# Kernel optimization log

Hardware: AMD Instinct MI355X
Metric: run time of the kernel (lower is better)

## Reference

```python
import jax, jax.numpy as jnp
import numpy as np

D = 4          # subsample stride for quantized refs
R = 6          # local search radius
P = 2 * R + 1  # 13
N = P * P      # 169
C = 32         # one-hot classes
BETA = 50.0
SIG = 1.0      # gaussian kernel sigma for kernel_soft_argmax
MPR = 12       # memory_patch_R
MPP = 2 * MPR + 1  # 25
DIL_INT = 15


def bilinear_gather(img, ys, xs):
    # img (b,c,h,w); ys,xs (b,n,h,w) float pixel coords; zero padding outside.
    b, c, h, w = img.shape
    y0f = jnp.floor(ys); x0f = jnp.floor(xs)
    wy = ys - y0f; wx = xs - x0f
    y0 = y0f.astype(jnp.int32); x0 = x0f.astype(jnp.int32)
    imgf = img.reshape(b, c, h * w)

    def corner(yi, xi, wgt):
        valid = (yi >= 0) & (yi < h) & (xi >= 0) & (xi < w)
        idx = jnp.clip(yi, 0, h - 1) * w + jnp.clip(xi, 0, w - 1)  # (b,n,h,w)
        g = jax.vmap(lambda f, ix: f[:, ix])(imgf, idx)            # (b,c,n,h,w)
        return g * (wgt * valid)[:, None]

    return (corner(y0, x0, (1 - wy) * (1 - wx))
            + corner(y0, x0 + 1, (1 - wy) * wx)
            + corner(y0 + 1, x0, wy * (1 - wx))
            + corner(y0 + 1, x0 + 1, wy * wx))


def deform_im2col(img, offset):
    # img (b,c,h,w); offset (b,h,w,2) ordered (dx,dy); returns (b,c,N,h,w)
    b, c, h, w = img.shape
    n = jnp.arange(N)
    dy = (n // P - R).astype(jnp.float32)
    dx = (n % P - R).astype(jnp.float32)
    yy = jnp.arange(h, dtype=jnp.float32)[:, None]
    xx = jnp.arange(w, dtype=jnp.float32)[None, :]
    ys = yy[None, None] + offset[..., 1][:, None] + dy[None, :, None, None]
    xs = xx[None, None] + offset[..., 0][:, None] + dx[None, :, None, None]
    return bilinear_gather(img, ys, xs)


def local_corr(t, r, rad, dil):
    # SpatialCorrelationSampler(kernel_size=1, patch_size=2*rad+1, dilation_patch=dil)
    pad = rad * dil
    rp = jnp.pad(r, ((0, 0), (0, 0), (pad, pad), (pad, pad)))
    offs = jnp.arange(2 * rad + 1) * dil

    def dot(oy, ox):
        rs = jax.lax.dynamic_slice(rp, (0, 0, oy, ox), t.shape)
        return jnp.sum(t * rs, axis=1)  # (b,h,w)

    f = jax.vmap(lambda oy: jax.vmap(lambda ox: dot(oy, ox))(offs))(offs)  # (Pp,Pp,b,h,w)
    return jnp.transpose(f, (2, 0, 1, 3, 4))  # (b,Pp,Pp,h,w), axis1=dy, axis2=dx


def unfold(x, ksz, pad):
    # torch F.unfold: (b,c,h,w) -> (b,c,ksz*ksz,h*w), n = ky*ksz+kx, zero pad
    b, c, h, w = x.shape
    xp = jnp.pad(x, ((0, 0), (0, 0), (pad, pad), (pad, pad)))
    offs = jnp.arange(ksz)
    sl = jax.vmap(lambda oy: jax.vmap(
        lambda ox: jax.lax.dynamic_slice(xp, (0, 0, oy, ox), x.shape))(offs))(offs)
    return jnp.transpose(sl, (2, 3, 0, 1, 4, 5)).reshape(b, c, ksz * ksz, h * w)


def kernel_soft_argmax(corr):
    # corr (B, N, h, w): gaussian-weight then softmax(beta * .) over N
    k = jnp.arange(P, dtype=jnp.float32)
    ctr = (P - 1) / 2.0
    g = jnp.exp(-(((k[None, :] - ctr) ** 2) + ((k[:, None] - ctr) ** 2)) / (2 * SIG ** 2))
    return jax.nn.softmax(BETA * (g.reshape(1, N, 1, 1) * corr), axis=1)


def get_grid(corr):
    # corr (B, N, h, w) -> soft-argmax grid (B, h, w, 2) in normalized coords
    B, n, h, w = corr.shape
    # replicate the torch meshgrid variable swap in the original get_grid
    x_map = jnp.broadcast_to(jnp.linspace(-1.0, 1.0, w)[None, :], (h, w)).astype(jnp.float32)
    y_map = jnp.broadcast_to(jnp.linspace(-1.0, 1.0, h)[:, None], (h, w)).astype(jnp.float32)
    xg = unfold(x_map[None, None], P, R)[:, 0]  # (1,N,hw)
    yg = unfold(y_map[None, None], P, R)[:, 0]
    wgt = corr.reshape(B, n, h * w)
    wgt = wgt / jnp.sum(wgt, 1, keepdims=True)
    gx = (wgt * xg).sum(1).reshape(B, h, w, 1)
    gy = (wgt * yg).sum(1).reshape(B, h, w, 1)
    return jnp.concatenate([gx, gy], 3)


def forward(feats_r, feats_t, quantized_r, ref_index, current_ind):
    ref_list = [int(v) for v in np.asarray(ref_index)]  # static config
    cur = int(current_ind)
    nref = feats_r.shape[0]
    nsearch = len([x for x in ref_list if cur - x > DIL_INT])
    dirates = [min(4, (cur - x) // DIL_INT + 1) for x in ref_list if cur - x > DIL_INT]
    b, c, h, w = feats_t.shape

    mdy = jnp.arange(-MPR, MPR + 1, dtype=jnp.float32)
    corrs, offsets = [], []
    for si in range(nsearch):
        cc = local_corr(feats_t, feats_r[si], MPR, dirates[si])       # (b,25,25,h,w)
        cc = jax.nn.softmax(cc.reshape(b, MPP * MPP, h * w), axis=1)
        cc = cc.reshape(b, MPP, MPP, h, w)
        offx = jnp.einsum('bpqhw,q->bhw', cc, mdy)   # expectation of dx
        offy = jnp.einsum('bpqhw,p->bhw', cc, mdy)   # expectation of dy
        off = jnp.stack([offx, offy], -1) * float(dirates[si])        # (b,h,w,2)
        offsets.append(off)
        col0 = deform_im2col(feats_r[si], off)                        # (b,c,N,h,w)
        corrs.append(jnp.einsum('bchw,bcnhw->bnhw', feats_t, col0))
    for ind in range(nsearch, nref):
        corrs.append(local_corr(feats_t, feats_r[ind], R, 1).reshape(b, N, h, w))

    corr = jnp.concatenate(corrs, 0)                 # (b*nref, N, h, w)
    corr = kernel_soft_argmax(corr)
    corr = corr.reshape(b, 1, N * nref, h * w)
    grid = get_grid(corr.reshape(-1, N, h, w))       # (b*nref, h, w, 2)

    # prep: subsample ::D and one-hot single-channel label maps
    labels = quantized_r[:, :, 0, ::D, ::D]          # (nref, b, h, w)
    qr = (labels[:, :, None] == jnp.arange(C)[None, None, :, None, None]).astype(jnp.float32)

    cols = []
    for i in range(nsearch):
        cols.append(deform_im2col(qr[i], offsets[i]).reshape(b, C, N, h * w))
    for i in range(nsearch, nref):
        cols.append(unfold(qr[i], P, R))
    image_uf = jnp.concatenate(cols, 2)              # (b, C, N*nref, hw)

    out = jnp.einsum('bnl,bcnl->bcl', corr[:, 0], image_uf).reshape(b, C, h, w)
    return out, grid


def setup_inputs() -> dict:
    key = jax.random.key(0)
    k1, k2, k3 = jax.random.split(key, 3)
    feats_r = jax.random.normal(k1, (3, 1, 64, 64, 64), dtype=jnp.float32)
    feats_t = jax.random.normal(k2, (1, 64, 64, 64), dtype=jnp.float32)
    quantized_r = jax.random.randint(k3, (3, 1, 1, 256, 256), 0, C, dtype=jnp.int32)
    return {
        'feats_r': feats_r,
        'feats_t': feats_t,
        'quantized_r': quantized_r,
        'ref_index': np.arange(3),
        'current_ind': 16,
    }


def reference(feats_r, feats_t, quantized_r, ref_index, current_ind):
    return forward(feats_r, feats_t, quantized_r, ref_index, current_ind)
```

## Files before the change

kernel.cpp:

```cpp
#include <hip/hip_runtime.h>


#define NPIX 4096

__device__ __forceinline__ float pdot8(float4 t0, float4 t1, float4 a,
                                       float4 b) {
  float s0 = t0.x * a.x, s1 = t0.y * a.y, s2 = t0.z * a.z, s3 = t0.w * a.w;
  s0 = fmaf(t1.x, b.x, s0);
  s1 = fmaf(t1.y, b.y, s1);
  s2 = fmaf(t1.z, b.z, s2);
  s3 = fmaf(t1.w, b.w, s3);
  return (s0 + s1) + (s2 + s3);
}

__device__ __forceinline__ float red8_8(float p0, float p1, float p2,
                                        float p3, float p4, float p5,
                                        float p6, float p7, int tx) {
  bool o1 = tx & 1, o2 = tx & 2, o4 = tx & 4;
  float a = (o1 ? p1 : p0) + __shfl_xor(o1 ? p0 : p1, 1);
  float b = (o1 ? p3 : p2) + __shfl_xor(o1 ? p2 : p3, 1);
  float c = (o1 ? p5 : p4) + __shfl_xor(o1 ? p4 : p5, 1);
  float d = (o1 ? p7 : p6) + __shfl_xor(o1 ? p6 : p7, 1);
  float e = (o2 ? b : a) + __shfl_xor(o2 ? a : b, 2);
  float f = (o2 ? d : c) + __shfl_xor(o2 ? c : d, 2);
  return (o4 ? f : e) + __shfl_xor(o4 ? e : f, 4);
}

__device__ __forceinline__ float red8(float v) {
  v += __shfl_xor(v, 1);
  v += __shfl_xor(v, 2);
  v += __shfl_xor(v, 4);
  return v;
}

__device__ __forceinline__ float wredmax(float v) {
#pragma unroll
  for (int o = 32; o; o >>= 1) v = fmaxf(v, __shfl_down(v, o));
  return __shfl(v, 0);
}
__device__ __forceinline__ float wredsum(float v) {
#pragma unroll
  for (int o = 32; o; o >>= 1) v += __shfl_down(v, o);
  return __shfl(v, 0);
}

__global__ __launch_bounds__(256) void k_transpose(
    const float* __restrict__ ft, const float* __restrict__ fr,
    const int* __restrict__ q, float* __restrict__ tT, float* __restrict__ rT,
    unsigned char* __restrict__ lblp) {
  __shared__ float tile[64][65];
  int img = blockIdx.y;
  int pixBase = blockIdx.x * 64;
  const float* src = (img == 0) ? ft : fr + (img - 1) * (64 * NPIX);
  float* dst = (img == 0) ? tT : rT + (img - 1) * (64 * NPIX);
  int tid = threadIdx.x;
#pragma unroll
  for (int it = 0; it < 4; ++it) {
    int idx = it * 256 + tid;
    int c = idx >> 4;
    int p4 = (idx & 15) << 2;
    float4 v = *(const float4*)&src[c * NPIX + pixBase + p4];
    tile[p4 + 0][c] = v.x;
    tile[p4 + 1][c] = v.y;
    tile[p4 + 2][c] = v.z;
    tile[p4 + 3][c] = v.w;
  }
  __syncthreads();
#pragma unroll
  for (int it = 0; it < 4; ++it) {
    int idx = it * 256 + tid;
    int p = idx >> 4;
    int c4 = (idx & 15) << 2;
    float4 v = make_float4(tile[p][c4], tile[p][c4 + 1], tile[p][c4 + 2],
                           tile[p][c4 + 3]);
    *(float4*)&dst[(pixBase + p) * 64 + c4] = v;
  }
  if (img >= 1 && tid < 64) {
    int pix = pixBase + tid;
    lblp[(img - 1) * 4096 + pix] = (unsigned char)
        q[(img - 1) * 65536 + (pix >> 6) * 1024 + (pix & 63) * 4];
  }
}

__global__ __launch_bounds__(512, 4) void k_fused(
    const float* __restrict__ tT, const float* __restrict__ rT,
    const unsigned char* __restrict__ lblp, float* __restrict__ out,
    float* __restrict__ grid) {
  int xg = blockIdx.x, y = blockIdx.y, z = blockIdx.z;
  int x0 = (xg >> 1) * 16 + (xg & 1);
  int tid = threadIdx.x;
  int g8 = tid >> 3, tx = tid & 7;
  int w = tid >> 6, lane = tid & 63;

  __shared__ float cc1[8 * 636];
  __shared__ float D[8][196];
  __shared__ float P0[8][169];
  __shared__ float bins[8][33];

  if (tid < 264) ((float*)bins)[tid] = 0.f;

  const float4* tb = (const float4*)&tT[((y << 6) + x0) << 6];
  float4 t0a = tb[0 * 32 + 2 * tx], t0b = tb[0 * 32 + 2 * tx + 1];
  float4 t1a = tb[1 * 32 + 2 * tx], t1b = tb[1 * 32 + 2 * tx + 1];
  float4 t2a = tb[2 * 32 + 2 * tx], t2b = tb[2 * 32 + 2 * tx + 1];
  float4 t3a = tb[3 * 32 + 2 * tx], t3b = tb[3 * 32 + 2 * tx + 1];
  float4 t4a = tb[4 * 32 + 2 * tx], t4b = tb[4 * 32 + 2 * tx + 1];
  float4 t5a = tb[5 * 32 + 2 * tx], t5b = tb[5 * 32 + 2 * tx + 1];
  float4 t6a = tb[6 * 32 + 2 * tx], t6b = tb[6 * 32 + 2 * tx + 1];
  float4 t7a = tb[7 * 32 + 2 * tx], t7b = tb[7 * 32 + 2 * tx + 1];

  if (z == 0) {
    {
      int u = g8 & 31, oyb = g8 >> 5;
      int rx = x0 - 24 + 2 * u;
      bool cok = (unsigned)rx < 64u;
      int colB = min(max(rx, 0), 63) * 64 + tx * 8;
      int ox = u - tx;
      bool sok = (unsigned)ox < 25u;
#pragma unroll 4
      for (int r = 0; r < 13; ++r) {
        int oy = oyb + 2 * r;
        int ry = y + 2 * oy - 24;
        bool ok = cok & (oy < 25) & ((unsigned)ry < 64u);
        const float4* rp =
            (const float4*)&rT[min(max(ry, 0), 63) * 4096 + colB];
        float4 ra = rp[0], rb = rp[1];
        float v = red8_8(pdot8(t0a, t0b, ra, rb), pdot8(t1a, t1b, ra, rb),
                         pdot8(t2a, t2b, ra, rb), pdot8(t3a, t3b, ra, rb),
                         pdot8(t4a, t4b, ra, rb), pdot8(t5a, t5b, ra, rb),
                         pdot8(t6a, t6b, ra, rb), pdot8(t7a, t7b, ra, rb),
                         tx);
        v = ok ? v : 0.f;
        if (sok && (oy < 25)) cc1[tx * 636 + oy * 25 + ox] = v;
      }
    }
    __syncthreads();

    float offx, offy;
    {
      float vv[10];
      float m = -3e38f;
#pragma unroll
      for (int it = 0; it < 10; ++it) {
        unsigned o = lane + (it << 6);
        float v = (o < 625u) ? cc1[w * 636 + o] : -3e38f;
        vv[it] = v;
        m = fmaxf(m, v);
      }
      m = wredmax(m);
      float s = 0.f, sx = 0.f, sy = 0.f;
#pragma unroll
      for (int it = 0; it < 10; ++it) {
        unsigned o = lane + (it << 6);
        unsigned oy = o / 25u, ox = o - oy * 25u;
        float e = __expf(vv[it] - m);
        s += e;
        sx += e * (float)((int)ox - 12);
        sy += e * (float)((int)oy - 12);
      }
      s = wredsum(s);
      sx = wredsum(sx);
      sy = wredsum(sy);
      offx = 2.f * sx / s;
      offy = 2.f * sy / s;
    }

    float fy = floorf(offy), fx = floorf(offx);
    float wy = offy - fy, wx = offx - fx;
    float w00 = (1.f - wy) * (1.f - wx), w01 = (1.f - wy) * wx;
    float w10 = wy * (1.f - wx), w11 = wy * wx;
    int iy0 = y + (int)fy - 6;
    int ix0 = x0 + 2 * w + (int)fx - 6;

    {
      const float4* Tp = (const float4*)&tT[((y << 6) + x0 + 2 * w) << 6];
      float4 T0 = Tp[2 * tx], T1 = Tp[2 * tx + 1];
      int g3 = lane >> 3;
#pragma unroll 4
      for (int r = 0; r < 28; ++r) {
        int idx = g3 + (r << 3);
        int a = idx >> 4, b = idx & 15;
        int ry = iy0 + a, rx = ix0 + b;
        bool ok = (b < 14) & ((unsigned)ry < 64u) & ((unsigned)rx < 64u);
        const float4* rp = (const float4*)
            &rT[(min(max(ry, 0), 63) * 64 + min(max(rx, 0), 63)) * 64];
        float4 ra = rp[2 * tx], rb = rp[2 * tx + 1];
        float v = red8(pdot8(T0, T1, ra, rb));
        if (tx == 0 && b < 14) D[w][a * 14 + b] = ok ? v : 0.f;
      }
    }

    {
      int px = x0 + 2 * w, pix = (y << 6) + px;
      float sc[3];
      float m = -3e38f;
#pragma unroll
      for (int it = 0; it < 3; ++it) {
        unsigned o = lane + (it << 6);
        float scv = -3e38f;
        if (o < 169u) {
          unsigned i = o / 13u, j = o - i * 13u;
          float v = w00 * D[w][i * 14 + j] + w01 * D[w][i * 14 + j + 1] +
                    w10 * D[w][(i + 1) * 14 + j] +
                    w11 * D[w][(i + 1) * 14 + j + 1];
          float di = (float)(((int)i - 6) * ((int)i - 6) +
                             ((int)j - 6) * ((int)j - 6));
          scv = 50.f * __expf(-0.5f * di) * v;
        }
        sc[it] = scv;
        m = fmaxf(m, scv);
      }
      m = wredmax(m);
      float ee[3];
      float s = 0.f, gx = 0.f, gy = 0.f;
#pragma unroll
      for (int it = 0; it < 3; ++it) {
        unsigned o = lane + (it << 6);
        unsigned i = o / 13u, j = o - i * 13u;
        float e = __expf(sc[it] - m);
        ee[it] = e;
        int yy = y + (int)i - 6, xx = px + (int)j - 6;
        bool inb = (o < 169u) && (unsigned)yy < 64u && (unsigned)xx < 64u;
        s += e;
        gx += e * (inb ? (-1.f + (2.f / 63.f) * (float)xx) : 0.f);
        gy += e * (inb ? (-1.f + (2.f / 63.f) * (float)yy) : 0.f);
      }
      s = wredsum(s);
      gx = wredsum(gx);
      gy = wredsum(gy);
      float invS = 1.f / s;
#pragma unroll
      for (int it = 0; it < 3; ++it) {
        unsigned o = lane + (it << 6);
        if (o < 169u) P0[w][o] = ee[it] * invS;
      }
      if (lane == 0) {
        grid[pix * 2 + 0] = gx * invS;
        grid[pix * 2 + 1] = gy * invS;
      }
    }

    {
#pragma unroll
      for (int it = 0; it < 4; ++it) {
        int idx = lane + (it << 6);
        int a = idx >> 4, b = idx & 15;
        if (a < 14 && b < 14) {
          int ry = iy0 + a, rx = ix0 + b;
          if ((unsigned)ry < 64u && (unsigned)rx < 64u) {
            float wgt = 0.f;
            const float* crp = P0[w];
            if (a < 13) {
              if (b < 13) wgt = fmaf(w00, crp[a * 13 + b], wgt);
              if (b > 0) wgt = fmaf(w01, crp[a * 13 + b - 1], wgt);
            }
            if (a > 0) {
              if (b < 13) wgt = fmaf(w10, crp[(a - 1) * 13 + b], wgt);
              if (b > 0) wgt = fmaf(w11, crp[(a - 1) * 13 + b - 1], wgt);
            }
            if (wgt != 0.f) atomicAdd(&bins[w][lblp[ry * 64 + rx]], wgt);
          }
        }
      }
    }
    __syncthreads();
  } else {
    int k = z;
    const float* rb0 = rT + (k << 18);
    float (*cc2)[169] = (float(*)[169])cc1;
    {
      int u = g8 & 31, ib = g8 >> 5;
      int rx = x0 - 6 + u;
      bool cok = (unsigned)rx < 64u;
      int colB = min(max(rx, 0), 63) * 64 + tx * 8;
      int j = u - 2 * tx;
      bool sok = (unsigned)j < 13u;
#pragma unroll 4
      for (int r = 0; r < 7; ++r) {
        int i = ib + 2 * r;
        int ry = y + i - 6;
        bool ok = cok & (i < 13) & ((unsigned)ry < 64u);
        const float4* rp =
            (const float4*)&rb0[min(max(ry, 0), 63) * 4096 + colB];
        float4 ra = rp[0], rb = rp[1];
        float v = red8_8(pdot8(t0a, t0b, ra, rb), pdot8(t1a, t1b, ra, rb),
                         pdot8(t2a, t2b, ra, rb), pdot8(t3a, t3b, ra, rb),
                         pdot8(t4a, t4b, ra, rb), pdot8(t5a, t5b, ra, rb),
                         pdot8(t6a, t6b, ra, rb), pdot8(t7a, t7b, ra, rb),
                         tx);
        v = ok ? v : 0.f;
        if (sok && (i < 13)) cc2[tx][i * 13 + j] = v;
      }
    }
    __syncthreads();
    {
      int px = x0 + 2 * w, pix = (y << 6) + px;
      float sc[3];
      float m = -3e38f;
#pragma unroll
      for (int it = 0; it < 3; ++it) {
        unsigned o = lane + (it << 6);
        float scv = -3e38f;
        if (o < 169u) {
          unsigned i = o / 13u, j = o - i * 13u;
          float di = (float)(((int)i - 6) * ((int)i - 6) +
                             ((int)j - 6) * ((int)j - 6));
          scv = 50.f * __expf(-0.5f * di) * cc2[w][o];
        }
        sc[it] = scv;
        m = fmaxf(m, scv);
      }
      m = wredmax(m);
      float ee[3];
      float s = 0.f, gx = 0.f, gy = 0.f;
#pragma unroll
      for (int it = 0; it < 3; ++it) {
        unsigned o = lane + (it << 6);
        unsigned i = o / 13u, j = o - i * 13u;
        float e = __expf(sc[it] - m);
        ee[it] = e;
        int yy = y + (int)i - 6, xx = px + (int)j - 6;
        bool inb = (o < 169u) && (unsigned)yy < 64u && (unsigned)xx < 64u;
        s += e;
        gx += e * (inb ? (-1.f + (2.f / 63.f) * (float)xx) : 0.f);
        gy += e * (inb ? (-1.f + (2.f / 63.f) * (float)yy) : 0.f);
      }
      s = wredsum(s);
      gx = wredsum(gx);
      gy = wredsum(gy);
      float invS = 1.f / s;
#pragma unroll
      for (int it = 0; it < 3; ++it) {
        unsigned o = lane + (it << 6);
        if (o < 169u) {
          unsigned i = o / 13u, j = o - i * 13u;
          int yy = y + (int)i - 6, xx = px + (int)j - 6;
          if ((unsigned)yy < 64u && (unsigned)xx < 64u)
            atomicAdd(&bins[w][lblp[(k << 12) + yy * 64 + xx]],
                      ee[it] * invS);
        }
      }
      if (lane == 0) {
        grid[(k * NPIX + pix) * 2 + 0] = gx * invS;
        grid[(k * NPIX + pix) * 2 + 1] = gy * invS;
      }
    }
    __syncthreads();
  }

  if (tid < 256) {
    int pp = tid & 7, c = tid >> 3;
    atomicAdd(&out[c * NPIX + (y << 6) + x0 + 2 * pp], bins[pp][c]);
  }
}

extern "C" void kernel_launch(void* const* d_in, const int* in_sizes, int n_in,
                              void* d_out, int out_size, void* d_ws,
                              size_t ws_size, hipStream_t stream) {
  const float* fr = (const float*)d_in[0];
  const float* ft = (const float*)d_in[1];
  const int* q = (const int*)d_in[2];
  float* out = (float*)d_out;
  float* grid = out + 32 * NPIX;

  float* ws = (float*)d_ws;
  float* tT = ws;
  float* rT = ws + 262144;
  unsigned char* lblp = (unsigned char*)(ws + 1048576);

  hipMemsetAsync(out, 0, 32 * NPIX * sizeof(float), stream);
  k_transpose<<<dim3(64, 4), 256, 0, stream>>>(ft, fr, q, tT, rT, lblp);
  k_fused<<<dim3(8, 64, 3), 512, 0, stream>>>(tT, rT, lblp, out, grid);
}
```

Before: 61.45 us.

## Halve fused block to 4 pixels, double grid, fold output zeroing into transpose

The fused kernel now runs 256-thread blocks that each handle 4 pixels instead of 512-thread blocks handling 8, and the grid doubles to 16x64x3. The correlation reductions are reworked for 4 pixels per octet (red8_4), and the z>0 blocks now take contiguous pixel groups rather than strided ones. The output memset is dropped: zeroing moves into the transpose kernel, removing one launch. The goal is better occupancy and load balance with less shared memory per block, at the cost of more redundant reference loads per computed value and more atomics on the output.

```diff
diff --git a/kernel.cpp b/kernel.cpp
--- a/kernel.cpp
+++ b/kernel.cpp
@@ -13,17 +13,20 @@
   return (s0 + s1) + (s2 + s3);
 }
 
-__device__ __forceinline__ float red8_8(float p0, float p1, float p2,
-                                        float p3, float p4, float p5,
-                                        float p6, float p7, int tx) {
-  bool o1 = tx & 1, o2 = tx & 2, o4 = tx & 4;
-  float a = (o1 ? p1 : p0) + __shfl_xor(o1 ? p0 : p1, 1);
-  float b = (o1 ? p3 : p2) + __shfl_xor(o1 ? p2 : p3, 1);
-  float c = (o1 ? p5 : p4) + __shfl_xor(o1 ? p4 : p5, 1);
-  float d = (o1 ? p7 : p6) + __shfl_xor(o1 ? p6 : p7, 1);
-  float e = (o2 ? b : a) + __shfl_xor(o2 ? a : b, 2);
-  float f = (o2 ? d : c) + __shfl_xor(o2 ? c : d, 2);
-  return (o4 ? f : e) + __shfl_xor(o4 ? e : f, 4);
+__device__ __forceinline__ float red8_4(float p0, float p1, float p2,
+                                        float p3, int tx) {
+  p0 += __shfl_xor(p0, 4);
+  p1 += __shfl_xor(p1, 4);
+  p2 += __shfl_xor(p2, 4);
+  p3 += __shfl_xor(p3, 4);
+  int t2 = tx & 3;
+  bool o1 = t2 & 1, o2 = t2 & 2;
+  float x01 = __shfl_xor(o1 ? p0 : p1, 1);
+  float x23 = __shfl_xor(o1 ? p2 : p3, 1);
+  float sA = (o1 ? p1 : p0) + x01;
+  float sB = (o1 ? p3 : p2) + x23;
+  float z = __shfl_xor(o2 ? sA : sB, 2);
+  return o2 ? (sB + z) : (sA + z);
 }
 
 __device__ __forceinline__ float red8(float v) {
@@ -47,7 +50,7 @@
 __global__ __launch_bounds__(256) void k_transpose(
     const float* __restrict__ ft, const float* __restrict__ fr,
     const int* __restrict__ q, float* __restrict__ tT, float* __restrict__ rT,
-    unsigned char* __restrict__ lblp) {
+    unsigned char* __restrict__ lblp, float* __restrict__ out) {
   __shared__ float tile[64][65];
   int img = blockIdx.y;
   int pixBase = blockIdx.x * 64;
@@ -80,58 +83,57 @@
     lblp[(img - 1) * 4096 + pix] = (unsigned char)
         q[(img - 1) * 65536 + (pix >> 6) * 1024 + (pix & 63) * 4];
   }
-}
-
-__global__ __launch_bounds__(512, 4) void k_fused(
+  int gi = (blockIdx.y * 64 + blockIdx.x) * 256 + tid;
+  out[gi] = 0.f;
+  out[gi + 65536] = 0.f;
+}
+
+__global__ __launch_bounds__(256, 6) void k_fused(
     const float* __restrict__ tT, const float* __restrict__ rT,
     const unsigned char* __restrict__ lblp, float* __restrict__ out,
     float* __restrict__ grid) {
   int xg = blockIdx.x, y = blockIdx.y, z = blockIdx.z;
-  int x0 = (xg >> 1) * 16 + (xg & 1);
   int tid = threadIdx.x;
-  int g8 = tid >> 3, tx = tid & 7;
+  int g = tid >> 3, tx = tid & 7;
   int w = tid >> 6, lane = tid & 63;
 
-  __shared__ float cc1[8 * 636];
-  __shared__ float D[8][196];
-  __shared__ float P0[8][169];
-  __shared__ float bins[8][33];
-
-  if (tid < 264) ((float*)bins)[tid] = 0.f;
-
-  const float4* tb = (const float4*)&tT[((y << 6) + x0) << 6];
-  float4 t0a = tb[0 * 32 + 2 * tx], t0b = tb[0 * 32 + 2 * tx + 1];
-  float4 t1a = tb[1 * 32 + 2 * tx], t1b = tb[1 * 32 + 2 * tx + 1];
-  float4 t2a = tb[2 * 32 + 2 * tx], t2b = tb[2 * 32 + 2 * tx + 1];
-  float4 t3a = tb[3 * 32 + 2 * tx], t3b = tb[3 * 32 + 2 * tx + 1];
-  float4 t4a = tb[4 * 32 + 2 * tx], t4b = tb[4 * 32 + 2 * tx + 1];
-  float4 t5a = tb[5 * 32 + 2 * tx], t5b = tb[5 * 32 + 2 * tx + 1];
-  float4 t6a = tb[6 * 32 + 2 * tx], t6b = tb[6 * 32 + 2 * tx + 1];
-  float4 t7a = tb[7 * 32 + 2 * tx], t7b = tb[7 * 32 + 2 * tx + 1];
+  __shared__ float cc1[4 * 636];
+  __shared__ float D[4][196];
+  __shared__ float P0[4][169];
+  __shared__ float bins[4][33];
+
+  if (tid < 132) ((float*)bins)[tid] = 0.f;
+
+  int opix;
 
   if (z == 0) {
-    {
-      int u = g8 & 31, oyb = g8 >> 5;
+    int x0 = (xg >> 1) * 8 + (xg & 1);
+    opix = x0;
+    const float4* tb = (const float4*)&tT[((y << 6) + x0) << 6];
+    float4 t0a = tb[0 * 32 + 2 * tx], t0b = tb[0 * 32 + 2 * tx + 1];
+    float4 t1a = tb[1 * 32 + 2 * tx], t1b = tb[1 * 32 + 2 * tx + 1];
+    float4 t2a = tb[2 * 32 + 2 * tx], t2b = tb[2 * 32 + 2 * tx + 1];
+    float4 t3a = tb[3 * 32 + 2 * tx], t3b = tb[3 * 32 + 2 * tx + 1];
+
+    {
+      int u = g;
       int rx = x0 - 24 + 2 * u;
       bool cok = (unsigned)rx < 64u;
       int colB = min(max(rx, 0), 63) * 64 + tx * 8;
-      int ox = u - tx;
-      bool sok = (unsigned)ox < 25u;
-#pragma unroll 4
-      for (int r = 0; r < 13; ++r) {
-        int oy = oyb + 2 * r;
-        int ry = y + 2 * oy - 24;
-        bool ok = cok & (oy < 25) & ((unsigned)ry < 64u);
+      int ox = u - (tx & 3);
+      bool sok = (tx < 4) & ((unsigned)ox < 25u);
+#pragma unroll 2
+      for (int r = 0; r < 25; ++r) {
+        int ry = y + 2 * r - 24;
+        bool ok = cok & ((unsigned)ry < 64u);
         const float4* rp =
             (const float4*)&rT[min(max(ry, 0), 63) * 4096 + colB];
         float4 ra = rp[0], rb = rp[1];
-        float v = red8_8(pdot8(t0a, t0b, ra, rb), pdot8(t1a, t1b, ra, rb),
+        float v = red8_4(pdot8(t0a, t0b, ra, rb), pdot8(t1a, t1b, ra, rb),
                          pdot8(t2a, t2b, ra, rb), pdot8(t3a, t3b, ra, rb),
-                         pdot8(t4a, t4b, ra, rb), pdot8(t5a, t5b, ra, rb),
-                         pdot8(t6a, t6b, ra, rb), pdot8(t7a, t7b, ra, rb),
                          tx);
         v = ok ? v : 0.f;
-        if (sok && (oy < 25)) cc1[tx * 636 + oy * 25 + ox] = v;
+        if (sok) cc1[(tx & 3) * 636 + r * 25 + ox] = v;
       }
     }
     __syncthreads();
@@ -176,7 +178,7 @@
       const float4* Tp = (const float4*)&tT[((y << 6) + x0 + 2 * w) << 6];
       float4 T0 = Tp[2 * tx], T1 = Tp[2 * tx + 1];
       int g3 = lane >> 3;
-#pragma unroll 4
+#pragma unroll 2
       for (int r = 0; r < 28; ++r) {
         int idx = g3 + (r << 3);
         int a = idx >> 4, b = idx & 15;
@@ -266,35 +268,40 @@
     __syncthreads();
   } else {
     int k = z;
+    int x0c = xg * 4;
+    opix = -x0c - 1;
     const float* rb0 = rT + (k << 18);
     float (*cc2)[169] = (float(*)[169])cc1;
-    {
-      int u = g8 & 31, ib = g8 >> 5;
-      int rx = x0 - 6 + u;
-      bool cok = (unsigned)rx < 64u;
-      int colB = min(max(rx, 0), 63) * 64 + tx * 8;
-      int j = u - 2 * tx;
-      bool sok = (unsigned)j < 13u;
-#pragma unroll 4
+    const float4* tb = (const float4*)&tT[((y << 6) + x0c) << 6];
+    float4 t0a = tb[0 * 16 + 2 * tx], t0b = tb[0 * 16 + 2 * tx + 1];
+    float4 t1a = tb[1 * 16 + 2 * tx], t1b = tb[1 * 16 + 2 * tx + 1];
+    float4 t2a = tb[2 * 16 + 2 * tx], t2b = tb[2 * 16 + 2 * tx + 1];
+    float4 t3a = tb[3 * 16 + 2 * tx], t3b = tb[3 * 16 + 2 * tx + 1];
+
+    {
+#pragma unroll 2
       for (int r = 0; r < 7; ++r) {
-        int i = ib + 2 * r;
-        int ry = y + i - 6;
-        bool ok = cok & (i < 13) & ((unsigned)ry < 64u);
-        const float4* rp =
-            (const float4*)&rb0[min(max(ry, 0), 63) * 4096 + colB];
+        int idx = g + (r << 5);
+        int i = idx >> 4, u = idx & 15;
+        int ry = y + i - 6, rx = x0c - 6 + u;
+        bool ok = (i < 13) & ((unsigned)ry < 64u) & ((unsigned)rx < 64u);
+        const float4* rp = (const float4*)
+            &rb0[min(max(ry, 0), 63) * 4096 + min(max(rx, 0), 63) * 64 +
+                 tx * 8];
         float4 ra = rp[0], rb = rp[1];
-        float v = red8_8(pdot8(t0a, t0b, ra, rb), pdot8(t1a, t1b, ra, rb),
+        float v = red8_4(pdot8(t0a, t0b, ra, rb), pdot8(t1a, t1b, ra, rb),
                          pdot8(t2a, t2b, ra, rb), pdot8(t3a, t3b, ra, rb),
-                         pdot8(t4a, t4b, ra, rb), pdot8(t5a, t5b, ra, rb),
-                         pdot8(t6a, t6b, ra, rb), pdot8(t7a, t7b, ra, rb),
                          tx);
         v = ok ? v : 0.f;
-        if (sok && (i < 13)) cc2[tx][i * 13 + j] = v;
+        int j = u - (tx & 3);
+        if ((tx < 4) && (i < 13) && ((unsigned)j < 13u))
+          cc2[tx & 3][i * 13 + j] = v;
       }
     }
     __syncthreads();
-    {
-      int px = x0 + 2 * w, pix = (y << 6) + px;
+
+    {
+      int px = x0c + w, pix = (y << 6) + px;
       float sc[3];
       float m = -3e38f;
 #pragma unroll
@@ -348,9 +355,10 @@
     __syncthreads();
   }
 
-  if (tid < 256) {
-    int pp = tid & 7, c = tid >> 3;
-    atomicAdd(&out[c * NPIX + (y << 6) + x0 + 2 * pp], bins[pp][c]);
+  if (tid < 128) {
+    int pp = tid & 3, c = tid >> 2;
+    int px = (opix >= 0) ? (opix + 2 * pp) : (-opix - 1 + pp);
+    atomicAdd(&out[c * NPIX + (y << 6) + px], bins[pp][c]);
   }
 }
 
@@ -368,7 +376,6 @@
   float* rT = ws + 262144;
   unsigned char* lblp = (unsigned char*)(ws + 1048576);
 
-  hipMemsetAsync(out, 0, 32 * NPIX * sizeof(float), stream);
-  k_transpose<<<dim3(64, 4), 256, 0, stream>>>(ft, fr, q, tT, rT, lblp);
-  k_fused<<<dim3(8, 64, 3), 512, 0, stream>>>(tT, rT, lblp, out, grid);
-}
+  k_transpose<<<dim3(64, 4), 256, 0, stream>>>(ft, fr, q, tT, rT, lblp, out);
+  k_fused<<<dim3(16, 64, 3), 256, 0, stream>>>(tT, rT, lblp, out, grid);
+}
```

New measurement: 49.98 us. -18.7%, faster.
